# Performance work log

Hardware: AMD Instinct MI355X
Metric: run time of the kernel (lower is better)

The kernel has to match this reference:

```python
import jax, jax.numpy as jnp
import numpy as np

EPS = 1e-06

def _normalize_gates(G1, G2, G3):
    sum_abs = jnp.abs(G1) + jnp.abs(G2) + jnp.abs(G3)
    sum_abs = jnp.where(sum_abs == 0, EPS, sum_abs)
    mask = (sum_abs >= 1).astype(G1.dtype)
    keep = 1.0 - mask
    G1 = keep * G1 + mask * (G1 / sum_abs)
    G2 = keep * G2 + mask * (G2 / sum_abs)
    G3 = keep * G3 + mask * (G3 / sum_abs)
    return G1, G2, G3

def _propagate_left_to_right(x, G1, G2, G3):
    # x, G*: [B, C, H, W]; recurrence along W (horizontal=True, reverse=False).
    # h[:, :, i, t] = (1 - g1 - g2 - g3) * x[..., i, t]
    #              + g1 * h[..., i-1, t-1] + g2 * h[..., i, t-1] + g3 * h[..., i+1, t-1]
    # out-of-range rows contribute zero.
    def to_scan(a):  # [B,C,H,W] -> [W,B,C,H]
        return jnp.moveaxis(a, 3, 0)
    xs = (to_scan(x), to_scan(G1), to_scan(G2), to_scan(G3))
    B, C, H, W = x.shape
    h0 = jnp.zeros((B, C, H), dtype=x.dtype)

    def step(h_prev, inp):
        xt, g1, g2, g3 = inp  # each [B, C, H]
        up = jnp.concatenate([jnp.zeros_like(h_prev[:, :, :1]), h_prev[:, :, :-1]], axis=2)   # h_prev[i-1]
        dn = jnp.concatenate([h_prev[:, :, 1:], jnp.zeros_like(h_prev[:, :, :1])], axis=2)    # h_prev[i+1]
        h = (1.0 - g1 - g2 - g3) * xt + g1 * up + g2 * h_prev + g3 * dn
        return h, h

    _, hs = jax.lax.scan(step, h0, xs)  # hs: [W, B, C, H]
    return jnp.moveaxis(hs, 0, 3)

def setup_inputs() -> dict:
    key = jax.random.key(0)
    k1, k2, k3, k4 = jax.random.split(key, 4)
    shape = (8, 32, 256, 256)
    return {
        'x': jax.random.normal(k1, shape, dtype=jnp.float32),
        'G1': jax.random.normal(k2, shape, dtype=jnp.float32),
        'G2': jax.random.normal(k3, shape, dtype=jnp.float32),
        'G3': jax.random.normal(k4, shape, dtype=jnp.float32),
    }

def reference(x, G1, G2, G3):
    G1n, G2n, G3n = _normalize_gates(G1, G2, G3)
    return _propagate_left_to_right(x, G1n, G2n, G3n)
```

## Files before the change

### kernel.cpp

```cpp
#include <hip/hip_runtime.h>


#define HH 256
#define WW 256
#define CHUNK 16
#define NCHUNK (WW / CHUNK)

#define ELEM(v, k) ((k) == 0 ? (v).x : ((k) == 1 ? (v).y : ((k) == 2 ? (v).z : (v).w)))

extern "C" __global__ void __launch_bounds__(256, 1)
spn_lr_kernel(const float* __restrict__ xg, const float* __restrict__ g1g,
              const float* __restrict__ g2g, const float* __restrict__ g3g,
              float* __restrict__ outg) {
    const int tid = threadIdx.x;
    const size_t rowbase = (size_t)blockIdx.x * (size_t)(HH * WW) + (size_t)tid * WW;
    const float4* px = reinterpret_cast<const float4*>(xg + rowbase);
    const float4* p1 = reinterpret_cast<const float4*>(g1g + rowbase);
    const float4* p2 = reinterpret_cast<const float4*>(g2g + rowbase);
    const float4* p3 = reinterpret_cast<const float4*>(g3g + rowbase);
    float4* po = reinterpret_cast<float4*>(outg + rowbase);

    __shared__ float hb0[HH + 2];
    __shared__ float hb1[HH + 2];
    hb0[tid + 1] = 0.0f;
    hb1[tid + 1] = 0.0f;
    if (tid == 0) {
        hb0[0] = 0.0f; hb1[0] = 0.0f;
        hb0[HH + 1] = 0.0f; hb1[HH + 1] = 0.0f;
    }
    __syncthreads();

    float4 nx[4], n1[4], n2[4], n3[4];
#pragma unroll
    for (int j = 0; j < 4; ++j) {
        nx[j] = px[j]; n1[j] = p1[j]; n2[j] = p2[j]; n3[j] = p3[j];
    }

    float h = 0.0f;

#pragma unroll 1
    for (int tc = 0; tc < NCHUNK; ++tc) {
        float xs[CHUNK], as[CHUNK], c1[CHUNK], c2[CHUNK], c3[CHUNK];
#pragma unroll
        for (int j = 0; j < 4; ++j) {
            float4 vx = nx[j], v1 = n1[j], v2 = n2[j], v3 = n3[j];
#pragma unroll
            for (int k = 0; k < 4; ++k) {
                const int s = j * 4 + k;
                float A1 = ELEM(v1, k), A2 = ELEM(v2, k), A3 = ELEM(v3, k);
                float sa = fabsf(A1) + fabsf(A2) + fabsf(A3);
                sa = (sa == 0.0f) ? 1e-6f : sa;
                const float inv = 1.0f / sa;
                const bool m = (sa >= 1.0f);
                const float B1 = m ? A1 * inv : A1;
                const float B2 = m ? A2 * inv : A2;
                const float B3 = m ? A3 * inv : A3;
                xs[s] = ELEM(vx, k);
                c1[s] = B1; c2[s] = B2; c3[s] = B3;
                as[s] = 1.0f - B1 - B2 - B3;
            }
        }

        if (tc + 1 < NCHUNK) {
            const int o = (tc + 1) * 4;
#pragma unroll
            for (int j = 0; j < 4; ++j) {
                nx[j] = px[o + j]; n1[j] = p1[o + j];
                n2[j] = p2[o + j]; n3[j] = p3[o + j];
            }
        }

        float ho[CHUNK];
#pragma unroll
        for (int s = 0; s < CHUNK; ++s) {
            const float* rb = (s & 1) ? hb1 : hb0;
            float* wb = (s & 1) ? hb0 : hb1;
            const float up = rb[tid];
            const float dn = rb[tid + 2];
            const float hn = as[s] * xs[s] + c1[s] * up + c2[s] * h + c3[s] * dn;
            wb[tid + 1] = hn;
            ho[s] = hn;
            h = hn;
            asm volatile("s_waitcnt lgkmcnt(0)" ::: "memory");
            __builtin_amdgcn_s_barrier();
            asm volatile("" ::: "memory");
        }

#pragma unroll
        for (int j = 0; j < 4; ++j) {
            float4 v;
            v.x = ho[j * 4 + 0]; v.y = ho[j * 4 + 1];
            v.z = ho[j * 4 + 2]; v.w = ho[j * 4 + 3];
            po[tc * 4 + j] = v;
        }
    }
}

extern "C" void kernel_launch(void* const* d_in, const int* in_sizes, int n_in,
                              void* d_out, int out_size, void* d_ws, size_t ws_size,
                              hipStream_t stream) {
    const float* x  = (const float*)d_in[0];
    const float* G1 = (const float*)d_in[1];
    const float* G2 = (const float*)d_in[2];
    const float* G3 = (const float*)d_in[3];
    float* out = (float*)d_out;

    const int nplanes = in_sizes[0] / (HH * WW);
    spn_lr_kernel<<<dim3(nplanes), dim3(HH), 0, stream>>>(x, G1, G2, G3, out);
}
```

Baseline: 99.80 us.

## Process each plane with one wavefront using shuffles instead of LDS barriers

Each plane is now handled by a single 64-lane wavefront, with every lane owning four adjacent rows. Neighbour exchange between steps uses register shuffles instead of shared memory and a block-wide barrier per column. Loads are double-buffered two chunks ahead. The cost is 4x fewer threads: only 256 single-wave blocks, so far less latency hiding and memory parallelism on a large GPU. Per-lane row strides also make global accesses uncoalesced across lanes.

```diff
diff --git a/kernel.cpp b/kernel.cpp
--- a/kernel.cpp
+++ b/kernel.cpp
@@ -3,97 +3,114 @@
 
 #define HH 256
 #define WW 256
-#define CHUNK 16
-#define NCHUNK (WW / CHUNK)
+#define CH 4
+#define NCH (WW / CH)
 
 #define ELEM(v, k) ((k) == 0 ? (v).x : ((k) == 1 ? (v).y : ((k) == 2 ? (v).z : (v).w)))
+#define SETEL(v, k, val)                                                     \
+    do {                                                                     \
+        if ((k) == 0) (v).x = (val);                                         \
+        else if ((k) == 1) (v).y = (val);                                    \
+        else if ((k) == 2) (v).z = (val);                                    \
+        else (v).w = (val);                                                  \
+    } while (0)
 
-extern "C" __global__ void __launch_bounds__(256, 1)
-spn_lr_kernel(const float* __restrict__ xg, const float* __restrict__ g1g,
-              const float* __restrict__ g2g, const float* __restrict__ g3g,
-              float* __restrict__ outg) {
-    const int tid = threadIdx.x;
-    const size_t rowbase = (size_t)blockIdx.x * (size_t)(HH * WW) + (size_t)tid * WW;
-    const float4* px = reinterpret_cast<const float4*>(xg + rowbase);
-    const float4* p1 = reinterpret_cast<const float4*>(g1g + rowbase);
-    const float4* p2 = reinterpret_cast<const float4*>(g2g + rowbase);
-    const float4* p3 = reinterpret_cast<const float4*>(g3g + rowbase);
-    float4* po = reinterpret_cast<float4*>(outg + rowbase);
+extern "C" __global__ void __launch_bounds__(64, 1)
+spn_lr_wave(const float* __restrict__ xg, const float* __restrict__ g1g,
+            const float* __restrict__ g2g, const float* __restrict__ g3g,
+            float* __restrict__ outg) {
+    const int lane = threadIdx.x;
+    const size_t pbase = (size_t)blockIdx.x * (size_t)(HH * (WW / 4));
+    const size_t rb0 = pbase + (size_t)(4 * lane + 0) * (WW / 4);
+    const size_t rb1 = pbase + (size_t)(4 * lane + 1) * (WW / 4);
+    const size_t rb2 = pbase + (size_t)(4 * lane + 2) * (WW / 4);
+    const size_t rb3 = pbase + (size_t)(4 * lane + 3) * (WW / 4);
 
-    __shared__ float hb0[HH + 2];
-    __shared__ float hb1[HH + 2];
-    hb0[tid + 1] = 0.0f;
-    hb1[tid + 1] = 0.0f;
-    if (tid == 0) {
-        hb0[0] = 0.0f; hb1[0] = 0.0f;
-        hb0[HH + 1] = 0.0f; hb1[HH + 1] = 0.0f;
-    }
-    __syncthreads();
+    const float4* px = reinterpret_cast<const float4*>(xg);
+    const float4* p1 = reinterpret_cast<const float4*>(g1g);
+    const float4* p2 = reinterpret_cast<const float4*>(g2g);
+    const float4* p3 = reinterpret_cast<const float4*>(g3g);
+    float4* po = reinterpret_cast<float4*>(outg);
 
-    float4 nx[4], n1[4], n2[4], n3[4];
-#pragma unroll
-    for (int j = 0; j < 4; ++j) {
-        nx[j] = px[j]; n1[j] = p1[j]; n2[j] = p2[j]; n3[j] = p3[j];
+    float4 bxA[4], b1A[4], b2A[4], b3A[4];
+    float4 bxB[4], b1B[4], b2B[4], b3B[4];
+
+    {
+        bxA[0] = px[rb0 + 0]; bxA[1] = px[rb1 + 0]; bxA[2] = px[rb2 + 0]; bxA[3] = px[rb3 + 0];
+        b1A[0] = p1[rb0 + 0]; b1A[1] = p1[rb1 + 0]; b1A[2] = p1[rb2 + 0]; b1A[3] = p1[rb3 + 0];
+        b2A[0] = p2[rb0 + 0]; b2A[1] = p2[rb1 + 0]; b2A[2] = p2[rb2 + 0]; b2A[3] = p2[rb3 + 0];
+        b3A[0] = p3[rb0 + 0]; b3A[1] = p3[rb1 + 0]; b3A[2] = p3[rb2 + 0]; b3A[3] = p3[rb3 + 0];
+        bxB[0] = px[rb0 + 1]; bxB[1] = px[rb1 + 1]; bxB[2] = px[rb2 + 1]; bxB[3] = px[rb3 + 1];
+        b1B[0] = p1[rb0 + 1]; b1B[1] = p1[rb1 + 1]; b1B[2] = p1[rb2 + 1]; b1B[3] = p1[rb3 + 1];
+        b2B[0] = p2[rb0 + 1]; b2B[1] = p2[rb1 + 1]; b2B[2] = p2[rb2 + 1]; b2B[3] = p2[rb3 + 1];
+        b3B[0] = p3[rb0 + 1]; b3B[1] = p3[rb1 + 1]; b3B[2] = p3[rb2 + 1]; b3B[3] = p3[rb3 + 1];
     }
 
-    float h = 0.0f;
+    float h0 = 0.0f, h1 = 0.0f, h2 = 0.0f, h3 = 0.0f;
+
+#define DO_CHUNK(TC, BX, B1, B2, B3)                                          \
+    do {                                                                      \
+        const int tc_ = (TC);                                                 \
+          \
+        float xs[4][4], aa[4][4], c1[4][4], c2[4][4], c3[4][4];               \
+        _Pragma("unroll") for (int q = 0; q < 4; ++q) {                       \
+            float4 vx = BX[q], v1 = B1[q], v2 = B2[q], v3 = B3[q];            \
+            _Pragma("unroll") for (int k = 0; k < 4; ++k) {                   \
+                float A1 = ELEM(v1, k), A2 = ELEM(v2, k), A3 = ELEM(v3, k);   \
+                float sa = fabsf(A1) + fabsf(A2) + fabsf(A3);                 \
+                sa = (sa == 0.0f) ? 1e-6f : sa;                               \
+                const float inv = 1.0f / sa;                                  \
+                const bool m = (sa >= 1.0f);                                  \
+                const float Q1 = m ? A1 * inv : A1;                           \
+                const float Q2 = m ? A2 * inv : A2;                           \
+                const float Q3 = m ? A3 * inv : A3;                           \
+                xs[q][k] = ELEM(vx, k);                                       \
+                c1[q][k] = Q1; c2[q][k] = Q2; c3[q][k] = Q3;                  \
+                aa[q][k] = 1.0f - Q1 - Q2 - Q3;                               \
+            }                                                                 \
+        }                                                                     \
+                 \
+        if (tc_ + 2 < NCH) {                                                  \
+            const int o = tc_ + 2;                                            \
+            BX[0] = px[rb0 + o]; BX[1] = px[rb1 + o];                         \
+            BX[2] = px[rb2 + o]; BX[3] = px[rb3 + o];                         \
+            B1[0] = p1[rb0 + o]; B1[1] = p1[rb1 + o];                         \
+            B1[2] = p1[rb2 + o]; B1[3] = p1[rb3 + o];                         \
+            B2[0] = p2[rb0 + o]; B2[1] = p2[rb1 + o];                         \
+            B2[2] = p2[rb2 + o]; B2[3] = p2[rb3 + o];                         \
+            B3[0] = p3[rb0 + o]; B3[1] = p3[rb1 + o];                         \
+            B3[2] = p3[rb2 + o]; B3[3] = p3[rb3 + o];                         \
+        }                                                                     \
+                               \
+        float4 o0, o1, o2, o3;                                                \
+        _Pragma("unroll") for (int k = 0; k < 4; ++k) {                       \
+            float up = __shfl_up(h3, 1);                                      \
+            float dn = __shfl_down(h0, 1);                                    \
+            up = (lane == 0) ? 0.0f : up;                                     \
+            dn = (lane == 63) ? 0.0f : dn;                                    \
+            const float t0 = aa[0][k] * xs[0][k] + c1[0][k] * up +            \
+                             c2[0][k] * h0 + c3[0][k] * h1;                   \
+            const float t1 = aa[1][k] * xs[1][k] + c1[1][k] * h0 +            \
+                             c2[1][k] * h1 + c3[1][k] * h2;                   \
+            const float t2 = aa[2][k] * xs[2][k] + c1[2][k] * h1 +            \
+                             c2[2][k] * h2 + c3[2][k] * h3;                   \
+            const float t3 = aa[3][k] * xs[3][k] + c1[3][k] * h2 +            \
+                             c2[3][k] * h3 + c3[3][k] * dn;                   \
+            h0 = t0; h1 = t1; h2 = t2; h3 = t3;                               \
+            SETEL(o0, k, t0); SETEL(o1, k, t1);                               \
+            SETEL(o2, k, t2); SETEL(o3, k, t3);                               \
+        }                                                                     \
+                              \
+        po[rb0 + tc_] = o0; po[rb1 + tc_] = o1;                               \
+        po[rb2 + tc_] = o2; po[rb3 + tc_] = o3;                               \
+    } while (0)
 
 #pragma unroll 1
-    for (int tc = 0; tc < NCHUNK; ++tc) {
-        float xs[CHUNK], as[CHUNK], c1[CHUNK], c2[CHUNK], c3[CHUNK];
-#pragma unroll
-        for (int j = 0; j < 4; ++j) {
-            float4 vx = nx[j], v1 = n1[j], v2 = n2[j], v3 = n3[j];
-#pragma unroll
-            for (int k = 0; k < 4; ++k) {
-                const int s = j * 4 + k;
-                float A1 = ELEM(v1, k), A2 = ELEM(v2, k), A3 = ELEM(v3, k);
-                float sa = fabsf(A1) + fabsf(A2) + fabsf(A3);
-                sa = (sa == 0.0f) ? 1e-6f : sa;
-                const float inv = 1.0f / sa;
-                const bool m = (sa >= 1.0f);
-                const float B1 = m ? A1 * inv : A1;
-                const float B2 = m ? A2 * inv : A2;
-                const float B3 = m ? A3 * inv : A3;
-                xs[s] = ELEM(vx, k);
-                c1[s] = B1; c2[s] = B2; c3[s] = B3;
-                as[s] = 1.0f - B1 - B2 - B3;
-            }
-        }
-
-        if (tc + 1 < NCHUNK) {
-            const int o = (tc + 1) * 4;
-#pragma unroll
-            for (int j = 0; j < 4; ++j) {
-                nx[j] = px[o + j]; n1[j] = p1[o + j];
-                n2[j] = p2[o + j]; n3[j] = p3[o + j];
-            }
-        }
-
-        float ho[CHUNK];
-#pragma unroll
-        for (int s = 0; s < CHUNK; ++s) {
-            const float* rb = (s & 1) ? hb1 : hb0;
-            float* wb = (s & 1) ? hb0 : hb1;
-            const float up = rb[tid];
-            const float dn = rb[tid + 2];
-            const float hn = as[s] * xs[s] + c1[s] * up + c2[s] * h + c3[s] * dn;
-            wb[tid + 1] = hn;
-            ho[s] = hn;
-            h = hn;
-            asm volatile("s_waitcnt lgkmcnt(0)" ::: "memory");
-            __builtin_amdgcn_s_barrier();
-            asm volatile("" ::: "memory");
-        }
-
-#pragma unroll
-        for (int j = 0; j < 4; ++j) {
-            float4 v;
-            v.x = ho[j * 4 + 0]; v.y = ho[j * 4 + 1];
-            v.z = ho[j * 4 + 2]; v.w = ho[j * 4 + 3];
-            po[tc * 4 + j] = v;
-        }
+    for (int t = 0; t < NCH; t += 2) {
+        DO_CHUNK(t, bxA, b1A, b2A, b3A);
+        DO_CHUNK(t + 1, bxB, b1B, b2B, b3B);
     }
+#undef DO_CHUNK
 }
 
 extern "C" void kernel_launch(void* const* d_in, const int* in_sizes, int n_in,
@@ -106,5 +123,5 @@
     float* out = (float*)d_out;
 
     const int nplanes = in_sizes[0] / (HH * WW);
-    spn_lr_kernel<<<dim3(nplanes), dim3(HH), 0, stream>>>(x, G1, G2, G3, out);
+    spn_lr_wave<<<dim3(nplanes), dim3(64), 0, stream>>>(x, G1, G2, G3, out);
 }
```

After: 310.0 us. 3.11x slower.

## Use one wavefront per plane with register rows and shuffle-based neighbor exchange

Applied to the files above, without the earlier changes.

Replaces the 256-thread block with a single 64-lane wavefront per plane, each lane handling four adjacent rows in registers. Neighbor rows are exchanged with wave shuffles instead of shared memory plus a block barrier at every column step. Loads for the next 16-column chunk are interleaved quarter by quarter with compute. The cost is a quarter as many threads per plane (256 waves total on the GPU) and heavy register use from the 80 float4 arrays, which limits latency hiding for global memory.

```diff
diff --git a/kernel.cpp b/kernel.cpp
--- a/kernel.cpp
+++ b/kernel.cpp
@@ -3,97 +3,115 @@
 
 #define HH 256
 #define WW 256
-#define CHUNK 16
-#define NCHUNK (WW / CHUNK)
 
-#define ELEM(v, k) ((k) == 0 ? (v).x : ((k) == 1 ? (v).y : ((k) == 2 ? (v).z : (v).w)))
+#define EL(v, k) ((k) == 0 ? (v).x : ((k) == 1 ? (v).y : ((k) == 2 ? (v).z : (v).w)))
+#define SETEL(v, k, val)                                                     \
+    do {                                                                     \
+        if ((k) == 0) (v).x = (val);                                         \
+        else if ((k) == 1) (v).y = (val);                                    \
+        else if ((k) == 2) (v).z = (val);                                    \
+        else (v).w = (val);                                                  \
+    } while (0)
 
-extern "C" __global__ void __launch_bounds__(256, 1)
-spn_lr_kernel(const float* __restrict__ xg, const float* __restrict__ g1g,
-              const float* __restrict__ g2g, const float* __restrict__ g3g,
-              float* __restrict__ outg) {
-    const int tid = threadIdx.x;
-    const size_t rowbase = (size_t)blockIdx.x * (size_t)(HH * WW) + (size_t)tid * WW;
-    const float4* px = reinterpret_cast<const float4*>(xg + rowbase);
-    const float4* p1 = reinterpret_cast<const float4*>(g1g + rowbase);
-    const float4* p2 = reinterpret_cast<const float4*>(g2g + rowbase);
-    const float4* p3 = reinterpret_cast<const float4*>(g3g + rowbase);
-    float4* po = reinterpret_cast<float4*>(outg + rowbase);
+extern "C" __global__ void __launch_bounds__(64, 1)
+spn_lr_reg(const float* __restrict__ xg, const float* __restrict__ g1g,
+           const float* __restrict__ g2g, const float* __restrict__ g3g,
+           float* __restrict__ outg) {
+    const int lane = threadIdx.x;
+    const size_t off =
+        (size_t)blockIdx.x * (size_t)(HH * WW) + (size_t)(4 * lane) * WW;
+    const float* bx = xg + off;
+    const float* b1 = g1g + off;
+    const float* b2 = g2g + off;
+    const float* b3 = g3g + off;
+    float* bo = outg + off;
 
-    __shared__ float hb0[HH + 2];
-    __shared__ float hb1[HH + 2];
-    hb0[tid + 1] = 0.0f;
-    hb1[tid + 1] = 0.0f;
-    if (tid == 0) {
-        hb0[0] = 0.0f; hb1[0] = 0.0f;
-        hb0[HH + 1] = 0.0f; hb1[HH + 1] = 0.0f;
-    }
-    __syncthreads();
+    float4 Sx[4][4], S1[4][4], S2[4][4], S3[4][4];
+    float4 o[4][4];
 
-    float4 nx[4], n1[4], n2[4], n3[4];
 #pragma unroll
-    for (int j = 0; j < 4; ++j) {
-        nx[j] = px[j]; n1[j] = p1[j]; n2[j] = p2[j]; n3[j] = p3[j];
+    for (int r = 0; r < 4; ++r) {
+#pragma unroll
+        for (int c = 0; c < 4; ++c) {
+            Sx[r][c] = *reinterpret_cast<const float4*>(bx + r * WW + c * 4);
+            S1[r][c] = *reinterpret_cast<const float4*>(b1 + r * WW + c * 4);
+            S2[r][c] = *reinterpret_cast<const float4*>(b2 + r * WW + c * 4);
+            S3[r][c] = *reinterpret_cast<const float4*>(b3 + r * WW + c * 4);
+        }
     }
 
-    float h = 0.0f;
+    float h0 = 0.0f, h1 = 0.0f, h2 = 0.0f, h3 = 0.0f;
+
+#define ROWC(RA, HU, HC, HD, NV, C4, K)                                       \
+    do {                                                                      \
+        float A1 = EL(S1[RA][C4], K);                                         \
+        float A2 = EL(S2[RA][C4], K);                                         \
+        float A3 = EL(S3[RA][C4], K);                                         \
+        const float sa = fabsf(A1) + fabsf(A2) + fabsf(A3);                   \
+        const float inv = (sa >= 1.0f) ? (1.0f / sa) : 1.0f;                  \
+        A1 *= inv; A2 *= inv; A3 *= inv;                                      \
+        const float d = (1.0f - A1 - A2 - A3) * EL(Sx[RA][C4], K);            \
+        NV = fmaf(A1, HU, fmaf(A2, HC, fmaf(A3, HD, d)));                     \
+    } while (0)
+
+#define STEP(C4, K)                                                           \
+    do {                                                                      \
+        float up = __shfl_up(h3, 1);                                          \
+        float dn = __shfl_down(h0, 1);                                        \
+        if (lane == 0) up = 0.0f;                                             \
+        if (lane == 63) dn = 0.0f;                                            \
+        float n0, n1, n2, n3;                                                 \
+        ROWC(0, up, h0, h1, n0, C4, K);                                       \
+        ROWC(1, h0, h1, h2, n1, C4, K);                                       \
+        ROWC(2, h1, h2, h3, n2, C4, K);                                       \
+        ROWC(3, h2, h3, dn, n3, C4, K);                                       \
+        h0 = n0; h1 = n1; h2 = n2; h3 = n3;                                   \
+        SETEL(o[0][C4], K, n0);                                               \
+        SETEL(o[1][C4], K, n1);                                               \
+        SETEL(o[2][C4], K, n2);                                               \
+        SETEL(o[3][C4], K, n3);                                               \
+    } while (0)
+
+#define QUARTER(C4)                                                           \
+    do { STEP(C4, 0); STEP(C4, 1); STEP(C4, 2); STEP(C4, 3); } while (0)
+
+#define LOADQ(C4)                                                             \
+    do {                                                                      \
+        if (pre) {                                                            \
+            _Pragma("unroll") for (int r_ = 0; r_ < 4; ++r_) {                \
+                Sx[r_][C4] = *reinterpret_cast<const float4*>(                \
+                    bx + 16 + r_ * WW + (C4) * 4);                            \
+                S1[r_][C4] = *reinterpret_cast<const float4*>(                \
+                    b1 + 16 + r_ * WW + (C4) * 4);                            \
+                S2[r_][C4] = *reinterpret_cast<const float4*>(                \
+                    b2 + 16 + r_ * WW + (C4) * 4);                            \
+                S3[r_][C4] = *reinterpret_cast<const float4*>(                \
+                    b3 + 16 + r_ * WW + (C4) * 4);                            \
+            }                                                                 \
+        }                                                                     \
+    } while (0)
 
 #pragma unroll 1
-    for (int tc = 0; tc < NCHUNK; ++tc) {
-        float xs[CHUNK], as[CHUNK], c1[CHUNK], c2[CHUNK], c3[CHUNK];
+    for (int p = 0; p < 16; ++p) {
+        const bool pre = (p < 15);
+        QUARTER(0); LOADQ(0);
+        QUARTER(1); LOADQ(1);
+        QUARTER(2); LOADQ(2);
+        QUARTER(3); LOADQ(3);
 #pragma unroll
-        for (int j = 0; j < 4; ++j) {
-            float4 vx = nx[j], v1 = n1[j], v2 = n2[j], v3 = n3[j];
+        for (int r = 0; r < 4; ++r) {
 #pragma unroll
-            for (int k = 0; k < 4; ++k) {
-                const int s = j * 4 + k;
-                float A1 = ELEM(v1, k), A2 = ELEM(v2, k), A3 = ELEM(v3, k);
-                float sa = fabsf(A1) + fabsf(A2) + fabsf(A3);
-                sa = (sa == 0.0f) ? 1e-6f : sa;
-                const float inv = 1.0f / sa;
-                const bool m = (sa >= 1.0f);
-                const float B1 = m ? A1 * inv : A1;
-                const float B2 = m ? A2 * inv : A2;
-                const float B3 = m ? A3 * inv : A3;
-                xs[s] = ELEM(vx, k);
-                c1[s] = B1; c2[s] = B2; c3[s] = B3;
-                as[s] = 1.0f - B1 - B2 - B3;
+            for (int c = 0; c < 4; ++c) {
+                *reinterpret_cast<float4*>(bo + r * WW + c * 4) = o[r][c];
             }
         }
+        bx += 16; b1 += 16; b2 += 16; b3 += 16; bo += 16;
+    }
 
-        if (tc + 1 < NCHUNK) {
-            const int o = (tc + 1) * 4;
-#pragma unroll
-            for (int j = 0; j < 4; ++j) {
-                nx[j] = px[o + j]; n1[j] = p1[o + j];
-                n2[j] = p2[o + j]; n3[j] = p3[o + j];
-            }
-        }
-
-        float ho[CHUNK];
-#pragma unroll
-        for (int s = 0; s < CHUNK; ++s) {
-            const float* rb = (s & 1) ? hb1 : hb0;
-            float* wb = (s & 1) ? hb0 : hb1;
-            const float up = rb[tid];
-            const float dn = rb[tid + 2];
-            const float hn = as[s] * xs[s] + c1[s] * up + c2[s] * h + c3[s] * dn;
-            wb[tid + 1] = hn;
-            ho[s] = hn;
-            h = hn;
-            asm volatile("s_waitcnt lgkmcnt(0)" ::: "memory");
-            __builtin_amdgcn_s_barrier();
-            asm volatile("" ::: "memory");
-        }
-
-#pragma unroll
-        for (int j = 0; j < 4; ++j) {
-            float4 v;
-            v.x = ho[j * 4 + 0]; v.y = ho[j * 4 + 1];
-            v.z = ho[j * 4 + 2]; v.w = ho[j * 4 + 3];
-            po[tc * 4 + j] = v;
-        }
-    }
+#undef LOADQ
+#undef QUARTER
+#undef STEP
+#undef ROWC
 }
 
 extern "C" void kernel_launch(void* const* d_in, const int* in_sizes, int n_in,
@@ -106,5 +124,5 @@
     float* out = (float*)d_out;
 
     const int nplanes = in_sizes[0] / (HH * WW);
-    spn_lr_kernel<<<dim3(nplanes), dim3(HH), 0, stream>>>(x, G1, G2, G3, out);
+    spn_lr_reg<<<dim3(nplanes), dim3(64), 0, stream>>>(x, G1, G2, G3, out);
 }
```

Result: slower. 192.4 us (+92.8%).
